# Optimization experiments

Measured on AMD Instinct MI355X. Metric: run time of the kernel, lower is better.

## Reference

```python
import jax, jax.numpy as jnp
import numpy as np

N_QUBITS = 4
NUM_LAYERS = 2
DIM = 2 ** N_QUBITS  # statevector dimension = 16
BN_EPS = 1e-5

# PennyLane default.qubit: wire 0 = most significant bit of the basis-state index.
def _bit(i, q):
    return (i >> (N_QUBITS - 1 - q)) & 1

# Precomputed CNOT permutations: if control bit set, flip target bit.
def _cnot_perm(c, t):
    idx = np.arange(DIM)
    flipped = idx ^ (1 << (N_QUBITS - 1 - t))
    return jnp.asarray(np.where((idx >> (N_QUBITS - 1 - c)) & 1 == 1, flipped, idx))

_CNOT_PERMS = [_cnot_perm(q, q + 1) for q in range(N_QUBITS - 1)] + [_cnot_perm(N_QUBITS - 1, 0)]

# <Z_q> sign table: sign[i, q] = +1 if bit q of basis state i is 0, else -1.
_Z_SIGNS = jnp.asarray(np.array([[1.0 - 2.0 * _bit(i, q) for q in range(N_QUBITS)]
                                 for i in range(DIM)], dtype=np.float32))

def _ry(state, theta, q):
    # state: [B, DIM] complex64, theta: [B] float32 (per-sample angle)
    B = state.shape[0]
    left, right = 2 ** q, 2 ** (N_QUBITS - 1 - q)
    s = state.reshape(B, left, 2, right)
    c = jnp.cos(0.5 * theta)[:, None, None]
    sn = jnp.sin(0.5 * theta)[:, None, None]
    a, b = s[:, :, 0, :], s[:, :, 1, :]
    out = jnp.stack([c * a - sn * b, sn * a + c * b], axis=2)
    return out.reshape(B, DIM)

def _rz(state, theta, q):
    # theta: scalar (shared trainable param)
    B = state.shape[0]
    left, right = 2 ** q, 2 ** (N_QUBITS - 1 - q)
    s = state.reshape(B, left, 2, right)
    p0 = jnp.exp(-0.5j * theta)
    p1 = jnp.exp(0.5j * theta)
    out = jnp.stack([p0 * s[:, :, 0, :], p1 * s[:, :, 1, :]], axis=2)
    return out.reshape(B, DIM)

def _circuit(encoded, q_params):
    # encoded: [B, N_QUBITS] angles; batched 4-qubit statevector simulation
    B = encoded.shape[0]
    state = jnp.zeros((B, DIM), jnp.complex64).at[:, 0].set(1.0)
    for layer in range(NUM_LAYERS):
        for q in range(N_QUBITS):
            state = _ry(state, encoded[:, q], q)
            state = _rz(state, q_params[layer, q], q)
        for perm in _CNOT_PERMS:
            state = state[:, perm]
    probs = jnp.abs(state) ** 2            # [B, DIM] float32
    return probs @ _Z_SIGNS                # [B, N_QUBITS] expvals of PauliZ

def setup_inputs() -> dict:
    key = jax.random.key(0)
    ks = jax.random.split(key, 4)
    B = 131072
    return {
        "x": jax.random.normal(ks[0], (B, 1, 24, 24), jnp.float32),
        "enc_w": jax.random.normal(ks[1], (N_QUBITS, 16), jnp.float32),
        "enc_b": jax.random.normal(ks[2], (N_QUBITS,), jnp.float32),
        "q_params": jax.random.normal(ks[3], (NUM_LAYERS, N_QUBITS), jnp.float32),
        "bn_weight": jnp.ones((N_QUBITS,), jnp.float32),
        "bn_bias": jnp.zeros((N_QUBITS,), jnp.float32),
    }

def reference(x, enc_w, enc_b, q_params, bn_weight, bn_bias):
    B = x.shape[0]
    # avg_pool2d(x, 6): [B,1,24,24] -> [B,1,4,4] -> [B,16]
    pooled = x.reshape(B, 1, 4, 6, 4, 6).mean(axis=(3, 5)).reshape(B, 16)
    encoded = pooled @ enc_w.T + enc_b      # [B, N_QUBITS]
    z = _circuit(encoded, q_params)         # [B, N_QUBITS]
    # BatchNorm1d in training mode: batch stats, biased variance
    mean = z.mean(axis=0)
    var = z.var(axis=0)
    return (z - mean) / jnp.sqrt(var + BN_EPS) * bn_weight + bn_bias
```

## Files before the change

kernel.cpp:

```cpp
#include <hip/hip_runtime.h>
#include <math.h>

#define BN_EPS 1e-5f

__host__ __device__ constexpr int blk_of(int p) {
    return (p / 144) * 4 + ((p % 24) / 6);
}

__global__ __launch_bounds__(256, 2) void qfc_main_kernel(
    const float* __restrict__ x,
    const float* __restrict__ enc_w,
    const float* __restrict__ enc_b,
    const float* __restrict__ qp,
    float* __restrict__ zout,
    float* __restrict__ acc)
{
    __shared__ float tile[256 * 36];
    __shared__ float wpack[64];
    __shared__ float red[32];

    const int t = threadIdx.x;
    if (t < 64) {
        int j = t >> 2, q = t & 3;
        wpack[t] = enc_w[q * 16 + j] * (1.0f / 36.0f);
    }

    const long long b0 = (long long)blockIdx.x * 256;
    const float* xb = x + b0 * 576;
    const int lrow = t >> 3;
    const int lcol = (t & 7) << 2;

    float4 pref[8];
#pragma unroll
    for (int rr = 0; rr < 8; rr++) {
        int row = lrow + rr * 32;
        pref[rr] = *(const float4*)(xb + (long long)row * 576 + lcol);
    }

    float pooled[16];
#pragma unroll
    for (int j = 0; j < 16; j++) pooled[j] = 0.0f;

#pragma unroll
    for (int ck = 0; ck < 18; ck++) {
#pragma unroll
        for (int rr = 0; rr < 8; rr++) {
            int row = lrow + rr * 32;
            *(float4*)(&tile[row * 36 + lcol]) = pref[rr];
        }
        __syncthreads();
        if (ck < 17) {
#pragma unroll
            for (int rr = 0; rr < 8; rr++) {
                int row = lrow + rr * 32;
                pref[rr] = *(const float4*)(xb + (long long)row * 576 + (ck + 1) * 32 + lcol);
            }
        }
        const float* trow = &tile[t * 36];
#pragma unroll
        for (int kk = 0; kk < 32; kk += 4) {
            float4 xv = *(const float4*)(&trow[kk]);
            const int p = ck * 32 + kk;
            pooled[blk_of(p + 0)] += xv.x;
            pooled[blk_of(p + 1)] += xv.y;
            pooled[blk_of(p + 2)] += xv.z;
            pooled[blk_of(p + 3)] += xv.w;
        }
        __syncthreads();
    }

    float e0 = enc_b[0], e1 = enc_b[1], e2 = enc_b[2], e3 = enc_b[3];
#pragma unroll
    for (int j = 0; j < 16; j++) {
        float4 w = *(const float4*)(&wpack[j * 4]);
        float pj = pooled[j];
        e0 += pj * w.x; e1 += pj * w.y; e2 += pj * w.z; e3 += pj * w.w;
    }
    float enc[4] = {e0, e1, e2, e3};

    float sr[16], si[16];
#pragma unroll
    for (int i = 0; i < 16; i++) { sr[i] = (i == 0) ? 1.0f : 0.0f; si[i] = 0.0f; }

#pragma unroll
    for (int layer = 0; layer < 2; layer++) {
#pragma unroll
        for (int q = 0; q < 4; q++) {
            float s, c;
            __sincosf(0.5f * enc[q], &s, &c);
            float zs, zc;
            __sincosf(0.5f * qp[layer * 4 + q], &zs, &zc);
            const int m = 8 >> q;
#pragma unroll
            for (int i0 = 0; i0 < 16; i0++) {
                if (i0 & m) continue;
                const int i1 = i0 | m;
                float ar = sr[i0], ai = si[i0], br = sr[i1], bi = si[i1];
                float n0r = c * ar - s * br, n0i = c * ai - s * bi;
                float n1r = s * ar + c * br, n1i = s * ai + c * bi;
                sr[i0] = zc * n0r + zs * n0i;  si[i0] = zc * n0i - zs * n0r;
                sr[i1] = zc * n1r - zs * n1i;  si[i1] = zc * n1i + zs * n1r;
            }
        }
#pragma unroll
        for (int g = 0; g < 4; g++) {
            const int cmask = 8 >> g;
            const int tmask = 8 >> ((g + 1) & 3);
#pragma unroll
            for (int i = 0; i < 16; i++) {
                if ((i & cmask) && !(i & tmask)) {
                    const int j = i | tmask;
                    float tr = sr[i]; sr[i] = sr[j]; sr[j] = tr;
                    float ti = si[i]; si[i] = si[j]; si[j] = ti;
                }
            }
        }
    }

    float z0 = 0, z1 = 0, z2 = 0, z3 = 0;
#pragma unroll
    for (int i = 0; i < 16; i++) {
        float p = sr[i] * sr[i] + si[i] * si[i];
        z0 += (i & 8) ? -p : p;
        z1 += (i & 4) ? -p : p;
        z2 += (i & 2) ? -p : p;
        z3 += (i & 1) ? -p : p;
    }

    float4 zv; zv.x = z0; zv.y = z1; zv.z = z2; zv.w = z3;
    *(float4*)(&zout[(b0 + t) * 4]) = zv;

    float v[8] = {z0, z1, z2, z3, z0 * z0, z1 * z1, z2 * z2, z3 * z3};
#pragma unroll
    for (int i = 0; i < 8; i++) {
        float s = v[i];
#pragma unroll
        for (int off = 32; off > 0; off >>= 1)
            s += __shfl_xor(s, off, 64);
        v[i] = s;
    }
    const int wave = t >> 6, lane = t & 63;
    if (lane == 0) {
#pragma unroll
        for (int i = 0; i < 8; i++) red[wave * 8 + i] = v[i];
    }
    __syncthreads();
    if (t < 8) {
        float s = red[t] + red[8 + t] + red[16 + t] + red[24 + t];
        atomicAdd(&acc[t], s);
    }
}

__global__ __launch_bounds__(256) void qfc_bn_kernel(
    float* __restrict__ out, const float* __restrict__ acc,
    const float* __restrict__ bn_w, const float* __restrict__ bn_b, int B)
{
    const int b = blockIdx.x * 256 + threadIdx.x;
    if (b >= B) return;
    const float invB = 1.0f / (float)B;
    float m0 = acc[0] * invB, m1 = acc[1] * invB, m2 = acc[2] * invB, m3 = acc[3] * invB;
    float s0 = rsqrtf(fmaxf(acc[4] * invB - m0 * m0, 0.0f) + BN_EPS);
    float s1 = rsqrtf(fmaxf(acc[5] * invB - m1 * m1, 0.0f) + BN_EPS);
    float s2 = rsqrtf(fmaxf(acc[6] * invB - m2 * m2, 0.0f) + BN_EPS);
    float s3 = rsqrtf(fmaxf(acc[7] * invB - m3 * m3, 0.0f) + BN_EPS);
    float4 z = ((float4*)out)[b];
    z.x = (z.x - m0) * s0 * bn_w[0] + bn_b[0];
    z.y = (z.y - m1) * s1 * bn_w[1] + bn_b[1];
    z.z = (z.z - m2) * s2 * bn_w[2] + bn_b[2];
    z.w = (z.w - m3) * s3 * bn_w[3] + bn_b[3];
    ((float4*)out)[b] = z;
}

extern "C" void kernel_launch(void* const* d_in, const int* in_sizes, int n_in,
                              void* d_out, int out_size, void* d_ws, size_t ws_size,
                              hipStream_t stream) {
    const float* x     = (const float*)d_in[0];
    const float* enc_w = (const float*)d_in[1];
    const float* enc_b = (const float*)d_in[2];
    const float* qp    = (const float*)d_in[3];
    const float* bn_w  = (const float*)d_in[4];
    const float* bn_b  = (const float*)d_in[5];
    float* out = (float*)d_out;
    float* acc = (float*)d_ws;

    const int B = in_sizes[0] / 576;

    hipMemsetAsync(acc, 0, 8 * sizeof(float), stream);

    qfc_main_kernel<<<B / 256, 256, 0, stream>>>(x, enc_w, enc_b, qp, out, acc);
    qfc_bn_kernel<<<(B + 255) / 256, 256, 0, stream>>>(out, acc, bn_w, bn_b, B);
}
```

Measured before the change: 445.2 us.

## Split each image across 8 lanes, drop LDS tile, and spread BN atomics

Each image is now handled by 8 lanes. Every lane loads 3 contiguous rows (72 floats) straight from global memory into registers, which removes the LDS transpose tile and its barriers. Each lane reduces its rows into column-block sums, and a shuffle combines the partial encoder products across the 8 lanes. The quantum circuit is then computed redundantly by all 8 lanes. Each lane writes one output or squared statistic, and the BN atomics go to 8 slots chosen by block index to reduce contention. The cost is 8x redundant circuit ALU work in exchange for higher occupancy, no shared-memory staging, and coalesced loads.

```diff
diff --git a/kernel.cpp b/kernel.cpp
--- a/kernel.cpp
+++ b/kernel.cpp
@@ -3,11 +3,7 @@
 
 #define BN_EPS 1e-5f
 
-__host__ __device__ constexpr int blk_of(int p) {
-    return (p / 144) * 4 + ((p % 24) / 6);
-}
-
-__global__ __launch_bounds__(256, 2) void qfc_main_kernel(
+__global__ __launch_bounds__(256, 4) void qfc_main_kernel(
     const float* __restrict__ x,
     const float* __restrict__ enc_w,
     const float* __restrict__ enc_b,
@@ -15,68 +11,54 @@
     float* __restrict__ zout,
     float* __restrict__ acc)
 {
-    __shared__ float tile[256 * 36];
     __shared__ float wpack[64];
     __shared__ float red[32];
 
     const int t = threadIdx.x;
     if (t < 64) {
-        int j = t >> 2, q = t & 3;
-        wpack[t] = enc_w[q * 16 + j] * (1.0f / 36.0f);
+        int blk = t >> 2, q = t & 3;
+        wpack[t] = enc_w[q * 16 + blk] * (1.0f / 36.0f);
+    }
+    __syncthreads();
+
+    const int j = t & 7;
+    const long long img = (long long)blockIdx.x * 32 + (t >> 3);
+    const float* base = x + img * 576 + j * 72;
+
+    float4 v[18];
+#pragma unroll
+    for (int k = 0; k < 18; k++) v[k] = *(const float4*)(base + k * 4);
+
+    float colacc[4] = {0.f, 0.f, 0.f, 0.f};
+#pragma unroll
+    for (int k = 0; k < 18; k++) {
+        const float e[4] = {v[k].x, v[k].y, v[k].z, v[k].w};
+#pragma unroll
+        for (int ee = 0; ee < 4; ee++) {
+            const int q = k * 4 + ee;
+            const int cb = (q % 24) / 6;
+            colacc[cb] += e[ee];
+        }
     }
 
-    const long long b0 = (long long)blockIdx.x * 256;
-    const float* xb = x + b0 * 576;
-    const int lrow = t >> 3;
-    const int lcol = (t & 7) << 2;
-
-    float4 pref[8];
+    const int rb = j >> 1;
+    float4 pe = {0.f, 0.f, 0.f, 0.f};
 #pragma unroll
-    for (int rr = 0; rr < 8; rr++) {
-        int row = lrow + rr * 32;
-        pref[rr] = *(const float4*)(xb + (long long)row * 576 + lcol);
+    for (int cb = 0; cb < 4; cb++) {
+        float4 w4 = *(const float4*)(&wpack[(rb * 4 + cb) * 4]);
+        pe.x += colacc[cb] * w4.x;
+        pe.y += colacc[cb] * w4.y;
+        pe.z += colacc[cb] * w4.z;
+        pe.w += colacc[cb] * w4.w;
     }
-
-    float pooled[16];
 #pragma unroll
-    for (int j = 0; j < 16; j++) pooled[j] = 0.0f;
-
-#pragma unroll
-    for (int ck = 0; ck < 18; ck++) {
-#pragma unroll
-        for (int rr = 0; rr < 8; rr++) {
-            int row = lrow + rr * 32;
-            *(float4*)(&tile[row * 36 + lcol]) = pref[rr];
-        }
-        __syncthreads();
-        if (ck < 17) {
-#pragma unroll
-            for (int rr = 0; rr < 8; rr++) {
-                int row = lrow + rr * 32;
-                pref[rr] = *(const float4*)(xb + (long long)row * 576 + (ck + 1) * 32 + lcol);
-            }
-        }
-        const float* trow = &tile[t * 36];
-#pragma unroll
-        for (int kk = 0; kk < 32; kk += 4) {
-            float4 xv = *(const float4*)(&trow[kk]);
-            const int p = ck * 32 + kk;
-            pooled[blk_of(p + 0)] += xv.x;
-            pooled[blk_of(p + 1)] += xv.y;
-            pooled[blk_of(p + 2)] += xv.z;
-            pooled[blk_of(p + 3)] += xv.w;
-        }
-        __syncthreads();
+    for (int m = 1; m <= 4; m <<= 1) {
+        pe.x += __shfl_xor(pe.x, m, 64);
+        pe.y += __shfl_xor(pe.y, m, 64);
+        pe.z += __shfl_xor(pe.z, m, 64);
+        pe.w += __shfl_xor(pe.w, m, 64);
     }
-
-    float e0 = enc_b[0], e1 = enc_b[1], e2 = enc_b[2], e3 = enc_b[3];
-#pragma unroll
-    for (int j = 0; j < 16; j++) {
-        float4 w = *(const float4*)(&wpack[j * 4]);
-        float pj = pooled[j];
-        e0 += pj * w.x; e1 += pj * w.y; e2 += pj * w.z; e3 += pj * w.w;
-    }
-    float enc[4] = {e0, e1, e2, e3};
+    float enc[4] = {pe.x + enc_b[0], pe.y + enc_b[1], pe.z + enc_b[2], pe.w + enc_b[3]};
 
     float sr[16], si[16];
 #pragma unroll
@@ -109,9 +91,9 @@
 #pragma unroll
             for (int i = 0; i < 16; i++) {
                 if ((i & cmask) && !(i & tmask)) {
-                    const int j = i | tmask;
-                    float tr = sr[i]; sr[i] = sr[j]; sr[j] = tr;
-                    float ti = si[i]; si[i] = si[j]; si[j] = ti;
+                    const int jj = i | tmask;
+                    float tr = sr[i]; sr[i] = sr[jj]; sr[jj] = tr;
+                    float ti = si[i]; si[i] = si[jj]; si[jj] = ti;
                 }
             }
         }
@@ -127,27 +109,19 @@
         z3 += (i & 1) ? -p : p;
     }
 
-    float4 zv; zv.x = z0; zv.y = z1; zv.z = z2; zv.w = z3;
-    *(float4*)(&zout[(b0 + t) * 4]) = zv;
+    const float sel = (j & 2) ? ((j & 1) ? z3 : z2) : ((j & 1) ? z1 : z0);
+    if (j < 4) zout[img * 4 + j] = sel;
 
-    float v[8] = {z0, z1, z2, z3, z0 * z0, z1 * z1, z2 * z2, z3 * z3};
+    float bnv = (j < 4) ? sel : sel * sel;
 #pragma unroll
-    for (int i = 0; i < 8; i++) {
-        float s = v[i];
-#pragma unroll
-        for (int off = 32; off > 0; off >>= 1)
-            s += __shfl_xor(s, off, 64);
-        v[i] = s;
-    }
-    const int wave = t >> 6, lane = t & 63;
-    if (lane == 0) {
-#pragma unroll
-        for (int i = 0; i < 8; i++) red[wave * 8 + i] = v[i];
-    }
+    for (int m = 8; m <= 32; m <<= 1) bnv += __shfl_xor(bnv, m, 64);
+
+    const int lane = t & 63, wv = t >> 6;
+    if (lane < 8) red[wv * 8 + lane] = bnv;
     __syncthreads();
     if (t < 8) {
         float s = red[t] + red[8 + t] + red[16 + t] + red[24 + t];
-        atomicAdd(&acc[t], s);
+        atomicAdd(&acc[(blockIdx.x & 7) * 8 + t], s);
     }
 }
 
@@ -157,12 +131,20 @@
 {
     const int b = blockIdx.x * 256 + threadIdx.x;
     if (b >= B) return;
+    float sm[8];
+#pragma unroll
+    for (int i = 0; i < 8; i++) {
+        float s = 0.f;
+#pragma unroll
+        for (int g = 0; g < 8; g++) s += acc[g * 8 + i];
+        sm[i] = s;
+    }
     const float invB = 1.0f / (float)B;
-    float m0 = acc[0] * invB, m1 = acc[1] * invB, m2 = acc[2] * invB, m3 = acc[3] * invB;
-    float s0 = rsqrtf(fmaxf(acc[4] * invB - m0 * m0, 0.0f) + BN_EPS);
-    float s1 = rsqrtf(fmaxf(acc[5] * invB - m1 * m1, 0.0f) + BN_EPS);
-    float s2 = rsqrtf(fmaxf(acc[6] * invB - m2 * m2, 0.0f) + BN_EPS);
-    float s3 = rsqrtf(fmaxf(acc[7] * invB - m3 * m3, 0.0f) + BN_EPS);
+    float m0 = sm[0] * invB, m1 = sm[1] * invB, m2 = sm[2] * invB, m3 = sm[3] * invB;
+    float s0 = rsqrtf(fmaxf(sm[4] * invB - m0 * m0, 0.0f) + BN_EPS);
+    float s1 = rsqrtf(fmaxf(sm[5] * invB - m1 * m1, 0.0f) + BN_EPS);
+    float s2 = rsqrtf(fmaxf(sm[6] * invB - m2 * m2, 0.0f) + BN_EPS);
+    float s3 = rsqrtf(fmaxf(sm[7] * invB - m3 * m3, 0.0f) + BN_EPS);
     float4 z = ((float4*)out)[b];
     z.x = (z.x - m0) * s0 * bn_w[0] + bn_b[0];
     z.y = (z.y - m1) * s1 * bn_w[1] + bn_b[1];
@@ -185,8 +167,8 @@
 
     const int B = in_sizes[0] / 576;
 
-    hipMemsetAsync(acc, 0, 8 * sizeof(float), stream);
+    hipMemsetAsync(acc, 0, 64 * sizeof(float), stream);
 
-    qfc_main_kernel<<<B / 256, 256, 0, stream>>>(x, enc_w, enc_b, qp, out, acc);
+    qfc_main_kernel<<<B / 32, 256, 0, stream>>>(x, enc_w, enc_b, qp, out, acc);
     qfc_bn_kernel<<<(B + 255) / 256, 256, 0, stream>>>(out, acc, bn_w, bn_b, B);
 }
```

Result: faster. 413.3 us (-7.2%).
